# Kernel optimization log

Hardware: AMD Instinct MI355X
Metric: run time of the kernel (lower is better)

## Reference

```python
import jax, jax.numpy as jnp
import numpy as np

B, N, DIM = 32, 577, 768   # N = num_patches + 1
H, DH = 12, 64             # heads, dim_head; inner_dim = H*DH = 768
NEG = -987654321.0         # LSA diagonal mask value from the source


def setup_inputs() -> dict:
    key = jax.random.key(0)
    ks = jax.random.split(key, 5)
    inner = H * DH
    base_scale = DH ** -0.5
    return {
        "x": jax.random.normal(ks[0], (B, N, DIM), dtype=jnp.float32),
        "W_qkv": jax.random.normal(ks[1], (DIM, inner * 3), dtype=jnp.float32) * (DIM ** -0.5),
        "scale": base_scale * (1.0 + 0.01 * jax.random.normal(ks[2], (H,), dtype=jnp.float32)),
        "W_out": jax.random.normal(ks[3], (inner, DIM), dtype=jnp.float32) * (inner ** -0.5),
        "b_out": jnp.zeros((DIM,), dtype=jnp.float32),
    }


def reference(x, W_qkv, scale, W_out, b_out):
    b, n, _ = x.shape
    qkv = x @ W_qkv                                   # [b, n, 3*H*DH]
    q, k, v = jnp.split(qkv, 3, axis=-1)
    to_heads = lambda t: t.reshape(b, n, H, DH).transpose(0, 2, 1, 3)  # b h n d
    q, k, v = to_heads(q), to_heads(k), to_heads(v)
    # per-head learnable scale (LSA)
    dots = jnp.einsum('bhid,bhjd->bhij', q, k) * scale[None, :, None, None]
    # mask self-attention diagonal (eye scatter in the torch source)
    eye = jnp.eye(n, dtype=bool)
    dots = jnp.where(eye[None, None], NEG, dots)
    attn = jax.nn.softmax(dots, axis=-1)
    out = jnp.einsum('bhij,bhjd->bhid', attn, v)      # b h n d
    out = out.transpose(0, 2, 1, 3).reshape(b, n, H * DH)
    return out @ W_out + b_out
```

## Files before the change

### kernel.cpp

```cpp
#include <hip/hip_runtime.h>


typedef _Float16 half8  __attribute__((ext_vector_type(8)));
typedef _Float16 h4f    __attribute__((ext_vector_type(4)));
typedef __fp16   hv2    __attribute__((ext_vector_type(2)));
typedef __fp16   hv4    __attribute__((ext_vector_type(4)));
typedef float    floatx4 __attribute__((ext_vector_type(4)));

#define MTOT   18464
#define NEG_V  (-987654321.0f)
#define VTS    584

__device__ __forceinline__ void gl_lds16(const _Float16* g, _Float16* l) {
    __builtin_amdgcn_global_load_lds(
        (const __attribute__((address_space(1))) unsigned int*)g,
        (__attribute__((address_space(3))) unsigned int*)l,
        16, 0, 0);
}

__global__ __launch_bounds__(256) void cvt_x(const float* __restrict__ x,
                                             _Float16* __restrict__ x16) {
    const size_t idx = ((size_t)blockIdx.x * 256 + threadIdx.x) * 8;
    half8 h = {};
    if (idx < (size_t)MTOT * 768) {
        float4 a = *(const float4*)(x + idx);
        float4 b = *(const float4*)(x + idx + 4);
        h[0] = (_Float16)a.x; h[1] = (_Float16)a.y;
        h[2] = (_Float16)a.z; h[3] = (_Float16)a.w;
        h[4] = (_Float16)b.x; h[5] = (_Float16)b.y;
        h[6] = (_Float16)b.z; h[7] = (_Float16)b.w;
    }
    *(half8*)(x16 + idx) = h;
}

__global__ __launch_bounds__(256) void transpose_w(const float* __restrict__ src,
                                                   _Float16* __restrict__ dst,
                                                   int K, int Ncol) {
    __shared__ float tile[32][33];
    const int n0 = blockIdx.x * 32, k0 = blockIdx.y * 32;
    const int tx = threadIdx.x & 31, ty = threadIdx.x >> 5;
    for (int i = 0; i < 32; i += 8)
        tile[ty + i][tx] = src[(size_t)(k0 + ty + i) * Ncol + (n0 + tx)];
    __syncthreads();
    for (int i = 0; i < 32; i += 8)
        dst[(size_t)(n0 + ty + i) * K + (k0 + tx)] = (_Float16)tile[tx][ty + i];
}

__global__ __launch_bounds__(256, 4) void gemm_qkv(const _Float16* __restrict__ x16,
                                                   const _Float16* __restrict__ wT,
                                                   const float* __restrict__ scale,
                                                   _Float16* __restrict__ qg,
                                                   _Float16* __restrict__ kg,
                                                   _Float16* __restrict__ vT) {
    __shared__ _Float16 As[2][128 * 32];
    __shared__ _Float16 Bs[2][128 * 32];
    const unsigned orig = blockIdx.x;
    const unsigned xcd = orig & 7u, bidx = orig >> 3;
    const unsigned swz = (xcd < 2u ? xcd * 327u : 654u + (xcd - 2u) * 326u) + bidx;
    const unsigned mi = swz / 18u, ni = swz - mi * 18u;
    const int m0 = (int)mi * 128, n0 = (int)ni * 128;
    const int tid = threadIdx.x;
    const int lane = tid & 63, wv = tid >> 6;
    const int wrow = wv >> 1, wcol = wv & 1;
    const int lr = lane & 15, lq = lane >> 4;

    const int r1 = tid >> 2,        c1 = (((tid & 3) ^ ((r1 >> 1) & 3)) * 8);
    const int r2 = 64 + (tid >> 2), c2 = (((tid & 3) ^ ((r2 >> 1) & 3)) * 8);
    const int xc = (lq ^ ((lr >> 1) & 3)) * 8;

    floatx4 acc[4][4];
    const floatx4 fz = {0.f, 0.f, 0.f, 0.f};
    for (int i = 0; i < 4; ++i)
        for (int j = 0; j < 4; ++j) acc[i][j] = fz;

    #define STAGE_QKV(ki, bfx)                                                      \
        do {                                                                        \
            const int kk_ = (ki) * 32;                                              \
            gl_lds16(x16 + (size_t)(m0 + r1) * 768 + kk_ + c1, &As[bfx][wv*64*8]);  \
            gl_lds16(x16 + (size_t)(m0 + r2) * 768 + kk_ + c2,                      \
                     &As[bfx][(256 + wv*64) * 8]);                                  \
            gl_lds16(wT + (size_t)(n0 + r1) * 768 + kk_ + c1, &Bs[bfx][wv*64*8]);   \
            gl_lds16(wT + (size_t)(n0 + r2) * 768 + kk_ + c2,                       \
                     &Bs[bfx][(256 + wv*64) * 8]);                                  \
        } while (0)

    STAGE_QKV(0, 0);
    for (int ki = 0; ki < 24; ++ki) {
        const int bf = ki & 1;
        if (ki < 23) {
            STAGE_QKV(ki + 1, bf ^ 1);
            asm volatile("s_waitcnt vmcnt(4)" ::: "memory");
        } else {
            asm volatile("s_waitcnt vmcnt(0)" ::: "memory");
        }
        asm volatile("s_barrier" ::: "memory");

        half8 af[4], bfr[4];
        #pragma unroll
        for (int i = 0; i < 4; ++i)
            af[i] = *(const half8*)&As[bf][(wrow * 64 + i * 16 + lr) * 32 + xc];
        #pragma unroll
        for (int j = 0; j < 4; ++j)
            bfr[j] = *(const half8*)&Bs[bf][(wcol * 64 + j * 16 + lr) * 32 + xc];
        #pragma unroll
        for (int i = 0; i < 4; ++i)
            #pragma unroll
            for (int j = 0; j < 4; ++j)
                acc[i][j] = __builtin_amdgcn_mfma_f32_16x16x32_f16(af[i], bfr[j], acc[i][j], 0, 0, 0);

        asm volatile("s_waitcnt lgkmcnt(0)\n\ts_barrier" ::: "memory");
    }
    #undef STAGE_QKV

    const int cbase = n0 + wcol * 64;
    const int which = cbase / 768;
    const int h = (cbase - which * 768) >> 6;
    const float qsc = (which == 0) ? scale[h] * 1.4426950408889634f : 1.0f;
    #pragma unroll
    for (int j = 0; j < 4; ++j) {
        const int d = j * 16 + lr;
        #pragma unroll
        for (int i = 0; i < 4; ++i)
            #pragma unroll
            for (int r = 0; r < 4; ++r) {
                const int row = m0 + wrow * 64 + i * 16 + lq * 4 + r;
                if (row >= MTOT) continue;
                const unsigned bb = (unsigned)row / 577u;
                const unsigned nn = (unsigned)row - bb * 577u;
                const _Float16 val = (_Float16)(acc[i][j][r] * qsc);
                const size_t head = (size_t)(bb * 12 + h);
                if (which == 0)      qg[(head * 577 + nn) * 64 + d] = val;
                else if (which == 1) kg[(head * 577 + nn) * 64 + d] = val;
                else                 vT[(head * 64 + d) * VTS + nn] = val;
            }
    }
}

__global__ __launch_bounds__(256) void attn_kernel(const _Float16* __restrict__ qg,
                                                   const _Float16* __restrict__ kg,
                                                   const _Float16* __restrict__ vT,
                                                   _Float16* __restrict__ Og) {
    __shared__ __align__(16) _Float16 Ks[64 * 64];
    __shared__ __align__(16) _Float16 Vs[64 * 64];
    const unsigned orig = blockIdx.x;
    const unsigned swz = (orig & 7u) * 240u + (orig >> 3);
    const int qt = (int)(swz % 5u);
    const unsigned hb = swz / 5u;
    const int h = (int)(hb % 12u), b = (int)(hb / 12u);
    const int tid = threadIdx.x, lane = tid & 63, wv = tid >> 6;
    const int lr = lane & 15, lq = lane >> 4;
    const size_t head = (size_t)(b * 12 + h);
    const _Float16* qh = qg + head * 577 * 64;
    const _Float16* kh = kg + head * 577 * 64;
    const _Float16* vh = vT + head * 64 * VTS;
    const int q0 = qt * 128;
    const int xs = lq ^ (lr & 7), xs4 = xs ^ 4;

    half8 bq[2][2];
    #pragma unroll
    for (int st = 0; st < 2; ++st) {
        const int qi = q0 + st * 64 + wv * 16 + lr;
        const int qc = qi < 577 ? qi : 576;
        bq[st][0] = *(const half8*)(qh + (size_t)qc * 64 + lq * 8);
        bq[st][1] = *(const half8*)(qh + (size_t)qc * 64 + 32 + lq * 8);
    }

    const floatx4 fz = {0.f, 0.f, 0.f, 0.f};
    floatx4 ot[2][4];
    #pragma unroll
    for (int st = 0; st < 2; ++st)
        #pragma unroll
        for (int c = 0; c < 4; ++c) ot[st][c] = fz;
    float sacc[2] = {0.f, 0.f};

    for (int kt = 0; kt < 10; ++kt) {
        const int j0 = kt * 64;
        __syncthreads();
        #pragma unroll
        for (int t = 0; t < 2; ++t) {
            const int c = t * 256 + wv * 64 + lane;
            const int row = c >> 3, cl = (c & 7) ^ (row & 7);
            gl_lds16(kh + (size_t)(j0 + row) * 64 + cl * 8,
                     Ks + (t * 256 + wv * 64) * 8);
            gl_lds16(vh + (size_t)row * VTS + j0 + cl * 8,
                     Vs + (t * 256 + wv * 64) * 8);
        }
        __syncthreads();

        half8 ak[4][2];
        #pragma unroll
        for (int ct = 0; ct < 4; ++ct) {
            const int base = (ct * 16 + lr) * 64;
            ak[ct][0] = *(const half8*)&Ks[base + xs * 8];
            ak[ct][1] = *(const half8*)&Ks[base + xs4 * 8];
        }

        floatx4 s[2][4];
        #pragma unroll
        for (int st = 0; st < 2; ++st)
            #pragma unroll
            for (int ct = 0; ct < 4; ++ct) {
                floatx4 t = __builtin_amdgcn_mfma_f32_16x16x32_f16(ak[ct][0], bq[st][0], fz, 0, 0, 0);
                s[st][ct] = __builtin_amdgcn_mfma_f32_16x16x32_f16(ak[ct][1], bq[st][1], t, 0, 0, 0);
            }

        if (kt == 9) {
            #pragma unroll
            for (int st = 0; st < 2; ++st) {
                s[st][0][0] = (lq == 0) ? s[st][0][0] : -INFINITY;
                s[st][0][1] = -INFINITY; s[st][0][2] = -INFINITY; s[st][0][3] = -INFINITY;
                #pragma unroll
                for (int ct = 1; ct < 4; ++ct) {
                    s[st][ct][0] = -INFINITY; s[st][ct][1] = -INFINITY;
                    s[st][ct][2] = -INFINITY; s[st][ct][3] = -INFINITY;
                }
            }
        }
        #pragma unroll
        for (int st = 0; st < 2; ++st) {
            if (kt == qt * 2 + st) {
                #pragma unroll
                for (int ct = 0; ct < 4; ++ct)
                    if (ct == wv) {
                        #pragma unroll
                        for (int r = 0; r < 4; ++r)
                            if (lq * 4 + r == lr) s[st][ct][r] = -INFINITY;
                    }
            }
        }

        hv4 pk[2][4];
        #pragma unroll
        for (int st = 0; st < 2; ++st)
            #pragma unroll
            for (int ct = 0; ct < 4; ++ct) {
                const float p0 = __builtin_amdgcn_exp2f(s[st][ct][0]);
                const float p1 = __builtin_amdgcn_exp2f(s[st][ct][1]);
                const float p2 = __builtin_amdgcn_exp2f(s[st][ct][2]);
                const float p3 = __builtin_amdgcn_exp2f(s[st][ct][3]);
                sacc[st] += (p0 + p1) + (p2 + p3);
                const hv2 lo = __builtin_amdgcn_cvt_pkrtz(p0, p1);
                const hv2 hi = __builtin_amdgcn_cvt_pkrtz(p2, p3);
                pk[st][ct] = __builtin_shufflevector(lo, hi, 0, 1, 2, 3);
            }

        #pragma unroll
        for (int jc = 0; jc < 4; ++jc) {
            const int csv = ((jc << 1) | (lq >> 1)) ^ (lr & 7);
            #pragma unroll
            for (int ctd = 0; ctd < 4; ++ctd) {
                const hv4 av = *(const hv4*)&Vs[(ctd * 16 + lr) * 64 + csv * 8 + (lq & 1) * 4];
                #pragma unroll
                for (int st = 0; st < 2; ++st)
                    ot[st][ctd] = __builtin_amdgcn_mfma_f32_16x16x16f16(av, pk[st][jc], ot[st][ctd], 0, 0, 0);
            }
        }
    }

    #pragma unroll
    for (int st = 0; st < 2; ++st) {
        float l = sacc[st];
        l += __shfl_xor(l, 16, 64);
        l += __shfl_xor(l, 32, 64);
        const float linv = 1.f / l;
        const int i = q0 + st * 64 + wv * 16 + lr;
        if (i < 577) {
            #pragma unroll
            for (int ctd = 0; ctd < 4; ++ctd) {
                h4f ov;
                #pragma unroll
                for (int r = 0; r < 4; ++r) ov[r] = (_Float16)(ot[st][ctd][r] * linv);
                *(h4f*)(Og + ((size_t)(b * 577 + i)) * 768 + h * 64 + ctd * 16 + lq * 4) = ov;
            }
        }
    }
}

__global__ __launch_bounds__(256, 4) void gemm_out(const _Float16* __restrict__ Og,
                                                   const _Float16* __restrict__ wT,
                                                   const float* __restrict__ bias,
                                                   float* __restrict__ out) {
    __shared__ _Float16 As[2][128 * 32];
    __shared__ _Float16 Bs[2][128 * 32];
    const unsigned orig = blockIdx.x;
    const unsigned xcd = orig & 7u, bidx = orig >> 3;
    const unsigned swz = (xcd < 6u ? xcd * 109u : 654u + (xcd - 6u) * 108u) + bidx;
    const unsigned mi = swz / 6u, ni = swz - mi * 6u;
    const int m0 = (int)mi * 128, n0 = (int)ni * 128;
    const int tid = threadIdx.x;
    const int lane = tid & 63, wv = tid >> 6;
    const int wrow = wv >> 1, wcol = wv & 1;
    const int lr = lane & 15, lq = lane >> 4;

    const int r1 = tid >> 2,        c1 = (((tid & 3) ^ ((r1 >> 1) & 3)) * 8);
    const int r2 = 64 + (tid >> 2), c2 = (((tid & 3) ^ ((r2 >> 1) & 3)) * 8);
    const int xc = (lq ^ ((lr >> 1) & 3)) * 8;

    floatx4 acc[4][4];
    const floatx4 fz = {0.f, 0.f, 0.f, 0.f};
    for (int i = 0; i < 4; ++i)
        for (int j = 0; j < 4; ++j) acc[i][j] = fz;

    #define STAGE_OUT(ki, bfx)                                                      \
        do {                                                                        \
            const int kk_ = (ki) * 32;                                              \
            gl_lds16(Og + (size_t)(m0 + r1) * 768 + kk_ + c1, &As[bfx][wv*64*8]);   \
            gl_lds16(Og + (size_t)(m0 + r2) * 768 + kk_ + c2,                       \
                     &As[bfx][(256 + wv*64) * 8]);                                  \
            gl_lds16(wT + (size_t)(n0 + r1) * 768 + kk_ + c1, &Bs[bfx][wv*64*8]);   \
            gl_lds16(wT + (size_t)(n0 + r2) * 768 + kk_ + c2,                       \
                     &Bs[bfx][(256 + wv*64) * 8]);                                  \
        } while (0)

    STAGE_OUT(0, 0);
    for (int ki = 0; ki < 24; ++ki) {
        const int bf = ki & 1;
        if (ki < 23) {
            STAGE_OUT(ki + 1, bf ^ 1);
            asm volatile("s_waitcnt vmcnt(4)" ::: "memory");
        } else {
            asm volatile("s_waitcnt vmcnt(0)" ::: "memory");
        }
        asm volatile("s_barrier" ::: "memory");

        half8 af[4], bfr[4];
        #pragma unroll
        for (int i = 0; i < 4; ++i)
            af[i] = *(const half8*)&As[bf][(wrow * 64 + i * 16 + lr) * 32 + xc];
        #pragma unroll
        for (int j = 0; j < 4; ++j)
            bfr[j] = *(const half8*)&Bs[bf][(wcol * 64 + j * 16 + lr) * 32 + xc];
        #pragma unroll
        for (int i = 0; i < 4; ++i)
            #pragma unroll
            for (int j = 0; j < 4; ++j)
                acc[i][j] = __builtin_amdgcn_mfma_f32_16x16x32_f16(af[i], bfr[j], acc[i][j], 0, 0, 0);

        asm volatile("s_waitcnt lgkmcnt(0)\n\ts_barrier" ::: "memory");
    }
    #undef STAGE_OUT

    #pragma unroll
    for (int j = 0; j < 4; ++j) {
        const int c = n0 + wcol * 64 + j * 16 + lr;
        const float bv = bias[c];
        #pragma unroll
        for (int i = 0; i < 4; ++i)
            #pragma unroll
            for (int r = 0; r < 4; ++r) {
                const int row = m0 + wrow * 64 + i * 16 + lq * 4 + r;
                if (row < MTOT) out[(size_t)row * 768 + c] = acc[i][j][r] + bv;
            }
    }
}

extern "C" void kernel_launch(void* const* d_in, const int* in_sizes, int n_in,
                              void* d_out, int out_size, void* d_ws, size_t ws_size,
                              hipStream_t stream) {
    const float* x      = (const float*)d_in[0];
    const float* W_qkv  = (const float*)d_in[1];
    const float* scale  = (const float*)d_in[2];
    const float* W_out  = (const float*)d_in[3];
    const float* b_out  = (const float*)d_in[4];
    float* out = (float*)d_out;

    char* ws = (char*)d_ws;
    _Float16* x16   = (_Float16*)(ws);
    _Float16* Og    = x16;
    _Float16* qg    = (_Float16*)(ws + 28508160u);
    _Float16* kg    = (_Float16*)(ws + 28508160u + 28360704u);
    _Float16* vT    = (_Float16*)(ws + 28508160u + 2u * 28360704u);
    _Float16* WqkvT = (_Float16*)(ws + 28508160u + 2u * 28360704u + 28704768u);
    _Float16* WoutT = WqkvT + (size_t)2304 * 768;

    cvt_x<<<6960, 256, 0, stream>>>(x, x16);
    transpose_w<<<dim3(72, 24), 256, 0, stream>>>(W_qkv, WqkvT, 768, 2304);
    transpose_w<<<dim3(24, 24), 256, 0, stream>>>(W_out, WoutT, 768, 768);
    gemm_qkv<<<2610, 256, 0, stream>>>(x16, WqkvT, scale, qg, kg, vT);
    attn_kernel<<<1920, 256, 0, stream>>>(qg, kg, vT, Og);
    gemm_out<<<870, 256, 0, stream>>>(Og, WoutT, b_out, out);
}
```

Before: 355.1 us.

## Double-buffer K/V LDS tiles in attention with prefetch of next tile

```diff
diff --git a/kernel.cpp b/kernel.cpp
--- a/kernel.cpp
+++ b/kernel.cpp
@@ -140,8 +140,8 @@
                                                    const _Float16* __restrict__ kg,
                                                    const _Float16* __restrict__ vT,
                                                    _Float16* __restrict__ Og) {
-    __shared__ __align__(16) _Float16 Ks[64 * 64];
-    __shared__ __align__(16) _Float16 Vs[64 * 64];
+    __shared__ __align__(16) _Float16 Ks[2][64 * 64];
+    __shared__ __align__(16) _Float16 Vs[2][64 * 64];
     const unsigned orig = blockIdx.x;
     const unsigned swz = (orig & 7u) * 240u + (orig >> 3);
     const int qt = (int)(swz % 5u);
@@ -165,6 +165,23 @@
         bq[st][1] = *(const half8*)(qh + (size_t)qc * 64 + 32 + lq * 8);
     }
 
+    #define PREF(kt_, pb_)                                               \
+        do {                                                             \
+            const int j0_ = (kt_) * 64;                                  \
+            {   const int c_ = wv * 64 + lane;                           \
+                const int r_ = c_ >> 3, cl_ = (c_ & 7) ^ (r_ & 7);       \
+                gl_lds16(kh + (size_t)(j0_ + r_) * 64 + cl_ * 8,         \
+                         &Ks[pb_][(wv * 64) * 8]);                       \
+                gl_lds16(vh + (size_t)r_ * VTS + j0_ + cl_ * 8,          \
+                         &Vs[pb_][(wv * 64) * 8]);   }                   \
+            {   const int c_ = 256 + wv * 64 + lane;                     \
+                const int r_ = c_ >> 3, cl_ = (c_ & 7) ^ (r_ & 7);       \
+                gl_lds16(kh + (size_t)(j0_ + r_) * 64 + cl_ * 8,         \
+                         &Ks[pb_][(256 + wv * 64) * 8]);                 \
+                gl_lds16(vh + (size_t)r_ * VTS + j0_ + cl_ * 8,          \
+                         &Vs[pb_][(256 + wv * 64) * 8]);   }             \
+        } while (0)
+
     const floatx4 fz = {0.f, 0.f, 0.f, 0.f};
     floatx4 ot[2][4];
     #pragma unroll
@@ -173,26 +190,23 @@
         for (int c = 0; c < 4; ++c) ot[st][c] = fz;
     float sacc[2] = {0.f, 0.f};
 
+    PREF(0, 0);
     for (int kt = 0; kt < 10; ++kt) {
-        const int j0 = kt * 64;
-        __syncthreads();
-        #pragma unroll
-        for (int t = 0; t < 2; ++t) {
-            const int c = t * 256 + wv * 64 + lane;
-            const int row = c >> 3, cl = (c & 7) ^ (row & 7);
-            gl_lds16(kh + (size_t)(j0 + row) * 64 + cl * 8,
-                     Ks + (t * 256 + wv * 64) * 8);
-            gl_lds16(vh + (size_t)row * VTS + j0 + cl * 8,
-                     Vs + (t * 256 + wv * 64) * 8);
-        }
-        __syncthreads();
+        const int bf = kt & 1;
+        if (kt < 9) {
+            PREF(kt + 1, bf ^ 1);
+            asm volatile("s_waitcnt vmcnt(4)" ::: "memory");
+        } else {
+            asm volatile("s_waitcnt vmcnt(0)" ::: "memory");
+        }
+        asm volatile("s_barrier" ::: "memory");
 
         half8 ak[4][2];
         #pragma unroll
         for (int ct = 0; ct < 4; ++ct) {
             const int base = (ct * 16 + lr) * 64;
-            ak[ct][0] = *(const half8*)&Ks[base + xs * 8];
-            ak[ct][1] = *(const half8*)&Ks[base + xs4 * 8];
+            ak[ct][0] = *(const half8*)&Ks[bf][base + xs * 8];
+            ak[ct][1] = *(const half8*)&Ks[bf][base + xs4 * 8];
         }
 
         floatx4 s[2][4];
@@ -249,13 +263,16 @@
             const int csv = ((jc << 1) | (lq >> 1)) ^ (lr & 7);
             #pragma unroll
             for (int ctd = 0; ctd < 4; ++ctd) {
-                const hv4 av = *(const hv4*)&Vs[(ctd * 16 + lr) * 64 + csv * 8 + (lq & 1) * 4];
+                const hv4 av = *(const hv4*)&Vs[bf][(ctd * 16 + lr) * 64 + csv * 8 + (lq & 1) * 4];
                 #pragma unroll
                 for (int st = 0; st < 2; ++st)
                     ot[st][ctd] = __builtin_amdgcn_mfma_f32_16x16x16f16(av, pk[st][jc], ot[st][ctd], 0, 0, 0);
             }
         }
-    }
+
+        asm volatile("s_waitcnt lgkmcnt(0)\n\ts_barrier" ::: "memory");
+    }
+    #undef PREF
 
     #pragma unroll
     for (int st = 0; st < 2; ++st) {
```

Measured after the change: 346.3 us. 1.03x faster.
